# Performance work log

Measured on AMD Instinct MI355X. Metric: run time of the kernel, lower is better.

Reference implementation:

```python
import jax, jax.numpy as jnp
import numpy as np


def setup_inputs() -> dict:
    key = jax.random.key(0)
    k1, k2, k3 = jax.random.split(key, 3)
    B, H, F, O = 2048, 512, 128, 10
    inputs = jax.random.normal(k1, (B, F), dtype=jnp.float32)
    # centers ~ uniform(-1, 1) as in init_params
    centers = jax.random.uniform(k2, (H, F), dtype=jnp.float32, minval=-1.0, maxval=1.0)
    sigma = jnp.ones((1,), dtype=jnp.float32)
    W = jax.random.normal(k3, (O, H), dtype=jnp.float32) * (1.0 / np.sqrt(H))
    b = jnp.zeros((O,), dtype=jnp.float32)
    return {"inputs": inputs, "centers": centers, "sigma": sigma, "W": W, "b": b}


def reference(inputs, centers, sigma, W, b):
    # pairwise squared distances: [B, H, F] diff -> sum over F -> [B, H]
    diff = inputs[:, None, :] - centers[None, :, :]
    distances = jnp.sum(diff * diff, axis=-1)  # [B, H]
    rbf = jnp.exp(-distances / (2.0 * sigma[0] ** 2))  # [B, H]
    # linear: y = rbf @ W.T + b
    return rbf @ W.T + b
```

## Files before the change

kernel.cpp:

```cpp
#include <hip/hip_runtime.h>


constexpr int Fdim = 128;
constexpr int Hdim = 512;
constexpr int Odim = 10;
constexpr int BM   = 8;
constexpr int KC   = 16;
constexpr int NCH  = Fdim / KC;
constexpr int LDXT = 12;

__global__ __launch_bounds__(512, 1) void rbf_all(
    const float* __restrict__ x,
    const float* __restrict__ c,
    const float* __restrict__ sigmap,
    const float* __restrict__ W,
    const float* __restrict__ bias,
    float* __restrict__ out)
{
    __shared__ float c_s[2][KC][Hdim];
    __shared__ float xT[Fdim][LDXT];
    __shared__ float rbf_s[BM][Hdim];
    __shared__ float cn_tmp[4][Hdim];
    __shared__ float po_s[BM][8][Odim];
    __shared__ float xn_s[BM];

    const int tid  = threadIdx.x;
    const int lane = tid & 63;
    const int wave = tid >> 6;
    const int wr   = wave >> 2;
    const int wh   = wave & 3;
    const int row0 = blockIdx.x * BM;

    const float4* x4 = reinterpret_cast<const float4*>(x);
    const float4* c4 = reinterpret_cast<const float4*>(c);

    if (tid < 256) {
        int r  = tid >> 5;
        int fq = tid & 31;
        float4 v = x4[(size_t)(row0 + r) * (Fdim / 4) + fq];
        xT[4 * fq + 0][r] = v.x;
        xT[4 * fq + 1][r] = v.y;
        xT[4 * fq + 2][r] = v.z;
        xT[4 * fq + 3][r] = v.w;
        float s = v.x * v.x + v.y * v.y + v.z * v.z + v.w * v.w;
#pragma unroll
        for (int sft = 1; sft < 32; sft <<= 1) s += __shfl_xor(s, sft, 64);
        if (fq == 0) xn_s[r] = s;
    }

    const int fq = tid >> 7;
    const int hq = tid & 127;

    float4 pre[4];
    float cnp[4] = {0.0f, 0.0f, 0.0f, 0.0f};

#define CLOAD(k)                                                              \
    {                                                                         \
        _Pragma("unroll")                                                     \
        for (int i = 0; i < 4; ++i)                                           \
            pre[i] = c4[(size_t)(4 * hq + i) * (Fdim / 4) + (k) * 4 + fq];    \
    }

#define CWRITE(k)                                                             \
    {                                                                         \
        float a0[4] = {pre[0].x, pre[0].y, pre[0].z, pre[0].w};               \
        float a1[4] = {pre[1].x, pre[1].y, pre[1].z, pre[1].w};               \
        float a2[4] = {pre[2].x, pre[2].y, pre[2].z, pre[2].w};               \
        float a3[4] = {pre[3].x, pre[3].y, pre[3].z, pre[3].w};               \
        _Pragma("unroll")                                                     \
        for (int j = 0; j < 4; ++j) {                                         \
            float4 w4;                                                        \
            w4.x = a0[j]; w4.y = a1[j]; w4.z = a2[j]; w4.w = a3[j];           \
            *reinterpret_cast<float4*>(&c_s[(k) & 1][4 * fq + j][4 * hq]) = w4; \
        }                                                                     \
        cnp[0] += pre[0].x * pre[0].x + pre[0].y * pre[0].y +                 \
                  pre[0].z * pre[0].z + pre[0].w * pre[0].w;                  \
        cnp[1] += pre[1].x * pre[1].x + pre[1].y * pre[1].y +                 \
                  pre[1].z * pre[1].z + pre[1].w * pre[1].w;                  \
        cnp[2] += pre[2].x * pre[2].x + pre[2].y * pre[2].y +                 \
                  pre[2].z * pre[2].z + pre[2].w * pre[2].w;                  \
        cnp[3] += pre[3].x * pre[3].x + pre[3].y * pre[3].y +                 \
                  pre[3].z * pre[3].z + pre[3].w * pre[3].w;                  \
    }

    CLOAD(0); CWRITE(0); CLOAD(1);
    __syncthreads();

    float acc[4][2];
#pragma unroll
    for (int i = 0; i < 4; ++i) { acc[i][0] = 0.0f; acc[i][1] = 0.0f; }

    for (int k = 0; k < NCH; ++k) {
        if (k + 1 < NCH) CWRITE(k + 1);
        if (k + 2 < NCH) CLOAD(k + 2);

#pragma unroll
        for (int f = 0; f < KC; ++f) {
            float4 xv = *reinterpret_cast<const float4*>(&xT[k * KC + f][4 * wr]);
            float2 cv = *reinterpret_cast<const float2*>(
                &c_s[k & 1][f][wh * 128 + 2 * lane]);
            acc[0][0] = fmaf(xv.x, cv.x, acc[0][0]);
            acc[0][1] = fmaf(xv.x, cv.y, acc[0][1]);
            acc[1][0] = fmaf(xv.y, cv.x, acc[1][0]);
            acc[1][1] = fmaf(xv.y, cv.y, acc[1][1]);
            acc[2][0] = fmaf(xv.z, cv.x, acc[2][0]);
            acc[2][1] = fmaf(xv.z, cv.y, acc[2][1]);
            acc[3][0] = fmaf(xv.w, cv.x, acc[3][0]);
            acc[3][1] = fmaf(xv.w, cv.y, acc[3][1]);
        }
        __syncthreads();
    }
#undef CLOAD
#undef CWRITE

    float2 W2[Odim][4];
#pragma unroll
    for (int o = 0; o < Odim; ++o)
#pragma unroll
        for (int k = 0; k < 4; ++k)
            W2[o][k] = *reinterpret_cast<const float2*>(
                &W[o * Hdim + 2 * lane + 128 * k]);

#pragma unroll
    for (int i = 0; i < 4; ++i) cn_tmp[fq][4 * hq + i] = cnp[i];
    __syncthreads();

    const float sg    = sigmap[0];
    const float scale = -1.0f / (2.0f * sg * sg);
    {
        float2 cn;
        cn.x = 0.0f; cn.y = 0.0f;
#pragma unroll
        for (int q = 0; q < 4; ++q) {
            float2 t = *reinterpret_cast<const float2*>(
                &cn_tmp[q][wh * 128 + 2 * lane]);
            cn.x += t.x; cn.y += t.y;
        }
#pragma unroll
        for (int i = 0; i < 4; ++i) {
            float xn = xn_s[4 * wr + i];
            float2 rv;
            rv.x = __expf((xn + cn.x - 2.0f * acc[i][0]) * scale);
            rv.y = __expf((xn + cn.y - 2.0f * acc[i][1]) * scale);
            *reinterpret_cast<float2*>(&rbf_s[4 * wr + i][wh * 128 + 2 * lane]) = rv;
        }
    }
    __syncthreads();

    {
        const int row = wave;
        float po[Odim];
#pragma unroll
        for (int o = 0; o < Odim; ++o) po[o] = 0.0f;

#pragma unroll
        for (int k = 0; k < 4; ++k) {
            float2 rv = *reinterpret_cast<const float2*>(
                &rbf_s[row][2 * lane + 128 * k]);
#pragma unroll
            for (int o = 0; o < Odim; ++o) {
                po[o] = fmaf(rv.x, W2[o][k].x, po[o]);
                po[o] = fmaf(rv.y, W2[o][k].y, po[o]);
            }
        }
#pragma unroll
        for (int s = 1; s < 8; s <<= 1) {
#pragma unroll
            for (int o = 0; o < Odim; ++o)
                po[o] += __shfl_xor(po[o], s, 64);
        }
        if ((lane & 7) == 0) {
#pragma unroll
            for (int o = 0; o < Odim; ++o)
                po_s[row][lane >> 3][o] = po[o];
        }
    }
    __syncthreads();

    if (tid < BM * Odim) {
        int w = tid / Odim;
        int o = tid - w * Odim;
        float v = bias[o];
#pragma unroll
        for (int g = 0; g < 8; ++g) v += po_s[w][g][o];
        out[(size_t)(row0 + w) * Odim + o] = v;
    }
}

extern "C" void kernel_launch(void* const* d_in, const int* in_sizes, int n_in,
                              void* d_out, int out_size, void* d_ws, size_t ws_size,
                              hipStream_t stream) {
    const float* x  = (const float*)d_in[0];
    const float* c  = (const float*)d_in[1];
    const float* sg = (const float*)d_in[2];
    const float* W  = (const float*)d_in[3];
    const float* b  = (const float*)d_in[4];
    float* out      = (float*)d_out;

    const int B = in_sizes[0] / Fdim;

    rbf_all<<<B / BM, 512, 0, stream>>>(x, c, sg, W, b, out);
}
```

Before: 20.50 us.

## Coalesce center loads, move staging after compute, reduce center norms via shuffles

Center loads are remapped so four adjacent threads read one center row's contiguous 64 bytes, replacing the strided per-thread row pattern. The shared-memory writes become scalar transposed stores. The write of the next chunk and the prefetch now happen after each chunk's FMA loop, with a single barrier per iteration and none after the last. Center norms are reduced with two xor-shuffles into a single shared array instead of a 4-way shared partial-sum buffer. The risk is more LDS store instructions, possible bank conflicts on the scalar transposed writes, and less overlap between the global loads and compute.

```diff
diff --git a/kernel.cpp b/kernel.cpp
--- a/kernel.cpp
+++ b/kernel.cpp
@@ -20,7 +20,7 @@
     __shared__ float c_s[2][KC][Hdim];
     __shared__ float xT[Fdim][LDXT];
     __shared__ float rbf_s[BM][Hdim];
-    __shared__ float cn_tmp[4][Hdim];
+    __shared__ float cn_s[Hdim];
     __shared__ float po_s[BM][8][Odim];
     __shared__ float xn_s[BM];
 
@@ -33,6 +33,34 @@
 
     const float4* x4 = reinterpret_cast<const float4*>(x);
     const float4* c4 = reinterpret_cast<const float4*>(c);
+
+    const int sfq = tid & 3;
+    const int sh  = tid >> 2;
+
+    float4 pre[4];
+    float cnp[4] = {0.0f, 0.0f, 0.0f, 0.0f};
+
+#define CLOAD(k)                                                              \
+    {                                                                         \
+        _Pragma("unroll")                                                     \
+        for (int p = 0; p < 4; ++p)                                           \
+            pre[p] = c4[(size_t)(sh + 128 * p) * (Fdim / 4) + (k) * 4 + sfq]; \
+    }
+#define CWRITE(k)                                                             \
+    {                                                                         \
+        _Pragma("unroll")                                                     \
+        for (int p = 0; p < 4; ++p) {                                         \
+            float4 v = pre[p];                                                \
+            int h = sh + 128 * p;                                             \
+            c_s[(k) & 1][4 * sfq + 0][h] = v.x;                               \
+            c_s[(k) & 1][4 * sfq + 1][h] = v.y;                               \
+            c_s[(k) & 1][4 * sfq + 2][h] = v.z;                               \
+            c_s[(k) & 1][4 * sfq + 3][h] = v.w;                               \
+            cnp[p] += v.x * v.x + v.y * v.y + v.z * v.z + v.w * v.w;          \
+        }                                                                     \
+    }
+
+    CLOAD(0);
 
     if (tid < 256) {
         int r  = tid >> 5;
@@ -48,42 +76,8 @@
         if (fq == 0) xn_s[r] = s;
     }
 
-    const int fq = tid >> 7;
-    const int hq = tid & 127;
-
-    float4 pre[4];
-    float cnp[4] = {0.0f, 0.0f, 0.0f, 0.0f};
-
-#define CLOAD(k)                                                              \
-    {                                                                         \
-        _Pragma("unroll")                                                     \
-        for (int i = 0; i < 4; ++i)                                           \
-            pre[i] = c4[(size_t)(4 * hq + i) * (Fdim / 4) + (k) * 4 + fq];    \
-    }
-
-#define CWRITE(k)                                                             \
-    {                                                                         \
-        float a0[4] = {pre[0].x, pre[0].y, pre[0].z, pre[0].w};               \
-        float a1[4] = {pre[1].x, pre[1].y, pre[1].z, pre[1].w};               \
-        float a2[4] = {pre[2].x, pre[2].y, pre[2].z, pre[2].w};               \
-        float a3[4] = {pre[3].x, pre[3].y, pre[3].z, pre[3].w};               \
-        _Pragma("unroll")                                                     \
-        for (int j = 0; j < 4; ++j) {                                         \
-            float4 w4;                                                        \
-            w4.x = a0[j]; w4.y = a1[j]; w4.z = a2[j]; w4.w = a3[j];           \
-            *reinterpret_cast<float4*>(&c_s[(k) & 1][4 * fq + j][4 * hq]) = w4; \
-        }                                                                     \
-        cnp[0] += pre[0].x * pre[0].x + pre[0].y * pre[0].y +                 \
-                  pre[0].z * pre[0].z + pre[0].w * pre[0].w;                  \
-        cnp[1] += pre[1].x * pre[1].x + pre[1].y * pre[1].y +                 \
-                  pre[1].z * pre[1].z + pre[1].w * pre[1].w;                  \
-        cnp[2] += pre[2].x * pre[2].x + pre[2].y * pre[2].y +                 \
-                  pre[2].z * pre[2].z + pre[2].w * pre[2].w;                  \
-        cnp[3] += pre[3].x * pre[3].x + pre[3].y * pre[3].y +                 \
-                  pre[3].z * pre[3].z + pre[3].w * pre[3].w;                  \
-    }
-
-    CLOAD(0); CWRITE(0); CLOAD(1);
+    CWRITE(0);
+    CLOAD(1);
     __syncthreads();
 
     float acc[4][2];
@@ -91,9 +85,6 @@
     for (int i = 0; i < 4; ++i) { acc[i][0] = 0.0f; acc[i][1] = 0.0f; }
 
     for (int k = 0; k < NCH; ++k) {
-        if (k + 1 < NCH) CWRITE(k + 1);
-        if (k + 2 < NCH) CLOAD(k + 2);
-
 #pragma unroll
         for (int f = 0; f < KC; ++f) {
             float4 xv = *reinterpret_cast<const float4*>(&xT[k * KC + f][4 * wr]);
@@ -108,7 +99,11 @@
             acc[3][0] = fmaf(xv.w, cv.x, acc[3][0]);
             acc[3][1] = fmaf(xv.w, cv.y, acc[3][1]);
         }
-        __syncthreads();
+        if (k + 1 < NCH) {
+            CWRITE(k + 1);
+            if (k + 2 < NCH) CLOAD(k + 2);
+            __syncthreads();
+        }
     }
 #undef CLOAD
 #undef CWRITE
@@ -117,25 +112,27 @@
 #pragma unroll
     for (int o = 0; o < Odim; ++o)
 #pragma unroll
-        for (int k = 0; k < 4; ++k)
-            W2[o][k] = *reinterpret_cast<const float2*>(
-                &W[o * Hdim + 2 * lane + 128 * k]);
-
-#pragma unroll
-    for (int i = 0; i < 4; ++i) cn_tmp[fq][4 * hq + i] = cnp[i];
+        for (int kk = 0; kk < 4; ++kk)
+            W2[o][kk] = *reinterpret_cast<const float2*>(
+                &W[o * Hdim + 2 * lane + 128 * kk]);
+
+#pragma unroll
+    for (int p = 0; p < 4; ++p) {
+        float s = cnp[p];
+        s += __shfl_xor(s, 1, 64);
+        s += __shfl_xor(s, 2, 64);
+        cnp[p] = s;
+    }
+    if (sfq == 0) {
+#pragma unroll
+        for (int p = 0; p < 4; ++p) cn_s[sh + 128 * p] = cnp[p];
+    }
     __syncthreads();
 
     const float sg    = sigmap[0];
     const float scale = -1.0f / (2.0f * sg * sg);
     {
-        float2 cn;
-        cn.x = 0.0f; cn.y = 0.0f;
-#pragma unroll
-        for (int q = 0; q < 4; ++q) {
-            float2 t = *reinterpret_cast<const float2*>(
-                &cn_tmp[q][wh * 128 + 2 * lane]);
-            cn.x += t.x; cn.y += t.y;
-        }
+        float2 cn = *reinterpret_cast<const float2*>(&cn_s[wh * 128 + 2 * lane]);
 #pragma unroll
         for (int i = 0; i < 4; ++i) {
             float xn = xn_s[4 * wr + i];
@@ -154,13 +151,13 @@
         for (int o = 0; o < Odim; ++o) po[o] = 0.0f;
 
 #pragma unroll
-        for (int k = 0; k < 4; ++k) {
+        for (int kk = 0; kk < 4; ++kk) {
             float2 rv = *reinterpret_cast<const float2*>(
-                &rbf_s[row][2 * lane + 128 * k]);
+                &rbf_s[row][2 * lane + 128 * kk]);
 #pragma unroll
             for (int o = 0; o < Odim; ++o) {
-                po[o] = fmaf(rv.x, W2[o][k].x, po[o]);
-                po[o] = fmaf(rv.y, W2[o][k].y, po[o]);
+                po[o] = fmaf(rv.x, W2[o][kk].x, po[o]);
+                po[o] = fmaf(rv.y, W2[o][kk].y, po[o]);
             }
         }
 #pragma unroll
```

Result: faster. 19.16 us (-6.5%).
